# Kernel tuning notes

Hardware: AMD Instinct MI355X
Metric: run time of the kernel (lower is better)

Reference implementation:

```python
import jax, jax.numpy as jnp
import numpy as np

N_NODES = 100000


def gcn_conv(x, src, dst, W, b, n):
    # PyG GCNConv: add self-loops, symmetric deg^-1/2 normalization,
    # linear transform, scatter-add aggregation, bias.
    loops = jnp.arange(n, dtype=src.dtype)
    s = jnp.concatenate([src, loops])
    d = jnp.concatenate([dst, loops])
    deg = jax.ops.segment_sum(jnp.ones_like(s, dtype=x.dtype), d, num_segments=n)
    dinv = jnp.where(deg > 0, jax.lax.rsqrt(deg), 0.0)
    norm = dinv[s] * dinv[d]  # [E+N]
    h = x @ W  # [N, out]
    msgs = h[s] * norm[:, None]  # gather + scale, [E+N, out]
    out = jax.ops.segment_sum(msgs, d, num_segments=n)  # scatter-add
    return out + b


def setup_inputs() -> dict:
    key = jax.random.key(0)
    k1, k2, k3, k4 = jax.random.split(key, 4)
    n, e = N_NODES, 1600000
    cin, chid, cout = 256, 128, 64
    x = jax.random.normal(k1, (n, cin), dtype=jnp.float32)
    edge_index = jax.random.randint(k2, (2, e), 0, n, dtype=jnp.int64)
    W1 = jax.random.normal(k3, (cin, chid), dtype=jnp.float32) * (1.0 / np.sqrt(cin))
    b1 = jnp.zeros((chid,), dtype=jnp.float32)
    W2 = jax.random.normal(k4, (chid, cout), dtype=jnp.float32) * (1.0 / np.sqrt(chid))
    b2 = jnp.zeros((cout,), dtype=jnp.float32)
    return {"x": x, "edge_index": edge_index, "W1": W1, "b1": b1, "W2": W2, "b2": b2}


def reference(x, edge_index, W1, b1, W2, b2):
    n = x.shape[0]
    src, dst = edge_index[0], edge_index[1]
    h = gcn_conv(x, src, dst, W1, b1, n)
    h = jax.nn.relu(h)
    # dropout is identity in eval mode (training=False)
    out = gcn_conv(h, src, dst, W2, b2, n)
    return out
```

## Files before the change

### kernel.cpp

```cpp
#include <hip/hip_runtime.h>


constexpr int NB_SHIFT = 7;
constexpr int NB_MAX   = 1024;
constexpr int BCAP     = 4096;
constexpr int BHIST    = 256;

__global__ __launch_bounds__(256) void k_hist(const int* __restrict__ dst,
                                              int* __restrict__ ghist,
                                              int E, int NB, int epb) {
    __shared__ int h[NB_MAX];
    const int t = threadIdx.x;
    for (int b = t; b < NB; b += 256) h[b] = 0;
    __syncthreads();
    const int e0 = blockIdx.x * epb;
    const int e1 = min(E, e0 + epb);
    for (int e = e0 + t; e < e1; e += 256) atomicAdd(&h[dst[e] >> NB_SHIFT], 1);
    __syncthreads();
    for (int b = t; b < NB; b += 256) ghist[b * gridDim.x + blockIdx.x] = h[b];
}

template <int TPB>
__global__ void k_scanL1(const int* __restrict__ in, int* __restrict__ out,
                         int* __restrict__ bsum, int ntot) {
    __shared__ int s[TPB];
    const int t = threadIdx.x;
    const int g = blockIdx.x * TPB + t;
    int v = (g < ntot) ? in[g] : 0;
    s[t] = v;
    __syncthreads();
    #pragma unroll
    for (int d = 1; d < TPB; d <<= 1) {
        int x = (t >= d) ? s[t - d] : 0;
        __syncthreads();
        s[t] += x;
        __syncthreads();
    }
    if (g < ntot) out[g] = s[t] - v;
    if (t == TPB - 1) bsum[blockIdx.x] = s[t];
}

__global__ void k_scanL2(int* __restrict__ bsum, int nb) {
    __shared__ int s[512];
    const int t = threadIdx.x;
    int v = (t < nb) ? bsum[t] : 0;
    s[t] = v;
    __syncthreads();
    #pragma unroll
    for (int d = 1; d < 512; d <<= 1) {
        int x = (t >= d) ? s[t - d] : 0;
        __syncthreads();
        s[t] += x;
        __syncthreads();
    }
    if (t < nb) bsum[t] = s[t] - v;
}

__global__ __launch_bounds__(256) void k_scatter(const int* __restrict__ src,
                                                 const int* __restrict__ dst,
                                                 const int* __restrict__ scan,
                                                 const int* __restrict__ bsum,
                                                 int2* __restrict__ pairs,
                                                 int E, int NB, int epb) {
    __shared__ int cur[NB_MAX];
    const int t = threadIdx.x;
    const int B = gridDim.x;
    const int blk = blockIdx.x;
    for (int b = t; b < NB; b += 256) {
        int idx = b * B + blk;
        cur[b] = scan[idx] + bsum[idx >> 9];
    }
    __syncthreads();
    const int e0 = blk * epb;
    const int e1 = min(E, e0 + epb);
    for (int e = e0 + t; e < e1; e += 256) {
        int d = dst[e];
        int slot = atomicAdd(&cur[d >> NB_SHIFT], 1);
        pairs[slot] = make_int2(src[e], d);
    }
}

__global__ __launch_bounds__(256) void k_build(const int2* __restrict__ pairs,
                                               const int* __restrict__ scan,
                                               const int* __restrict__ bsum,
                                               int* __restrict__ srcs,
                                               int* __restrict__ off,
                                               float* __restrict__ dinv,
                                               int n, int E, int NB, int B) {
    __shared__ int h[128], loff[128], curs[128];
    __shared__ int sb[BCAP];
    const int t = threadIdx.x;
    const int bk = blockIdx.x;
    const int i0 = bk * B;
    const int base = scan[i0] + bsum[i0 >> 9];
    const int nextbase = (bk + 1 < NB) ? (scan[i0 + B] + bsum[(i0 + B) >> 9]) : E;
    const int count = nextbase - base;
    if (t < 128) h[t] = 0;
    __syncthreads();
    for (int e = t; e < count; e += 256) atomicAdd(&h[pairs[base + e].y & 127], 1);
    __syncthreads();
    if (t < 128) loff[t] = h[t];
    __syncthreads();
    #pragma unroll
    for (int d = 1; d < 128; d <<= 1) {
        int x = 0;
        if (t < 128 && t >= d) x = loff[t - d];
        __syncthreads();
        if (t < 128) loff[t] += x;
        __syncthreads();
    }
    if (t < 128) curs[t] = loff[t] - h[t];
    __syncthreads();
    for (int e = t; e < count; e += 256) {
        int2 p = pairs[base + e];
        int slot = atomicAdd(&curs[p.y & 127], 1);
        if (slot < BCAP) sb[slot] = p.x;
        else srcs[base + slot] = p.x;
    }
    __syncthreads();
    const int lim = min(count, BCAP);
    for (int e = t; e < lim; e += 256) srcs[base + e] = sb[e];
    const int node0 = bk << NB_SHIFT;
    if (t < 128) {
        int node = node0 + t;
        if (node < n) {
            off[node] = base + (loff[t] - h[t]);
            dinv[node] = rsqrtf((float)(h[t] + 1));
        }
    }
    if (bk == 0 && t == 0) off[n] = E;
}

template <int K, int N, int BM, int BK, int TM, int TN>
__global__ __launch_bounds__(256) void k_gemm(const float* __restrict__ A,
                                              const float* __restrict__ B,
                                              float* __restrict__ C, int M) {
    constexpr int BN = N;
    constexpr int NTX = BN / TN;
    __shared__ float As[BM][BK];
    __shared__ float Bs[BK][BN];
    const int t = threadIdx.x;
    const int tx = t % NTX;
    const int ty = t / NTX;
    const int row0 = blockIdx.x * BM;
    float acc[TM][TN] = {};
    for (int kc = 0; kc < K; kc += BK) {
        #pragma unroll
        for (int i = 0; i < BM * BK / (256 * 4); ++i) {
            int f = (t + i * 256) * 4;
            int r = f / BK, kq = f % BK;
            float4 v = make_float4(0.f, 0.f, 0.f, 0.f);
            if (row0 + r < M)
                v = *(const float4*)(A + (size_t)(row0 + r) * K + kc + kq);
            *(float4*)&As[r][kq] = v;
        }
        #pragma unroll
        for (int i = 0; i < BK * BN / (256 * 4); ++i) {
            int f = (t + i * 256) * 4;
            int r = f / BN, c = f % BN;
            *(float4*)&Bs[r][c] = *(const float4*)(B + (size_t)(kc + r) * N + c);
        }
        __syncthreads();
        #pragma unroll
        for (int kk = 0; kk < BK; ++kk) {
            float a[TM], b[TN];
            #pragma unroll
            for (int i = 0; i < TM; ++i) a[i] = As[ty * TM + i][kk];
            #pragma unroll
            for (int j = 0; j < TN; ++j) b[j] = Bs[kk][tx * TN + j];
            #pragma unroll
            for (int i = 0; i < TM; ++i)
                #pragma unroll
                for (int j = 0; j < TN; ++j)
                    acc[i][j] = fmaf(a[i], b[j], acc[i][j]);
        }
        __syncthreads();
    }
    #pragma unroll
    for (int i = 0; i < TM; ++i) {
        int r = row0 + ty * TM + i;
        if (r < M)
            *(float4*)(C + (size_t)r * N + tx * TN) = *(float4*)&acc[i][0];
    }
}

template <int C, bool RELU>
__global__ __launch_bounds__(256) void k_aggregate(
    const float* __restrict__ h, const int* __restrict__ off,
    const int* __restrict__ srcs, const float* __restrict__ dinv,
    const float* __restrict__ bias, float* __restrict__ out, int n) {
    __shared__ float2 stage[256];
    const int tid = threadIdx.x;
    const int lane = tid & 63;
    const int wbase = tid & ~63;
    int wid = (int)((blockIdx.x * (size_t)blockDim.x + tid) >> 6);
    if (wid >= n) return;
    const float di = dinv[wid];
    const int e0 = off[wid], e1 = off[wid + 1];
    if constexpr (C == 128) {
        const float2* hp = (const float2*)h;
        float2 acc = hp[(size_t)wid * 64 + lane];
        acc.x *= di * di;
        acc.y *= di * di;
        for (int e = e0; e < e1; e += 64) {
            int m = e1 - e;
            if (m > 64) m = 64;
            float2 pk = make_float2(0.f, 0.f);
            if (lane < m) {
                int s = srcs[e + lane];
                pk.x = __int_as_float(s);
                pk.y = dinv[s] * di;
            }
            stage[tid] = pk;
            #pragma unroll 4
            for (int j = 0; j < m; ++j) {
                float2 sw = stage[wbase + j];
                int sj = __float_as_int(sw.x);
                float wj = sw.y;
                float2 v = hp[(size_t)sj * 64 + lane];
                acc.x = fmaf(v.x, wj, acc.x);
                acc.y = fmaf(v.y, wj, acc.y);
            }
        }
        float2 bb = ((const float2*)bias)[lane];
        acc.x += bb.x;
        acc.y += bb.y;
        if (RELU) {
            acc.x = fmaxf(acc.x, 0.f);
            acc.y = fmaxf(acc.y, 0.f);
        }
        ((float2*)out)[(size_t)wid * 64 + lane] = acc;
    } else {
        float acc = h[(size_t)wid * C + lane] * di * di;
        for (int e = e0; e < e1; e += 64) {
            int m = e1 - e;
            if (m > 64) m = 64;
            float2 pk = make_float2(0.f, 0.f);
            if (lane < m) {
                int s = srcs[e + lane];
                pk.x = __int_as_float(s);
                pk.y = dinv[s] * di;
            }
            stage[tid] = pk;
            #pragma unroll 4
            for (int j = 0; j < m; ++j) {
                float2 sw = stage[wbase + j];
                int sj = __float_as_int(sw.x);
                float wj = sw.y;
                acc = fmaf(h[(size_t)sj * C + lane], wj, acc);
            }
        }
        acc += bias[lane];
        if (RELU) acc = fmaxf(acc, 0.f);
        out[(size_t)wid * C + lane] = acc;
    }
}

extern "C" void kernel_launch(void* const* d_in, const int* in_sizes, int n_in,
                              void* d_out, int out_size, void* d_ws, size_t ws_size,
                              hipStream_t stream) {
    const float* x  = (const float*)d_in[0];
    const int*   ei = (const int*)d_in[1];
    const float* W1 = (const float*)d_in[2];
    const float* b1 = (const float*)d_in[3];
    const float* W2 = (const float*)d_in[4];
    const float* b2 = (const float*)d_in[5];
    float* out = (float*)d_out;

    const int n = in_sizes[0] / 256;
    const int E = in_sizes[1] / 2;
    const int* src = ei;
    const int* dst = ei + E;

    const int NB  = (n + 127) >> NB_SHIFT;
    const int B   = BHIST;
    const int epb = (E + B - 1) / B;
    const int ntot = NB * B;
    const int gL1 = (ntot + 511) / 512;

    char* p = (char*)d_ws;
    auto alloc = [&](size_t bytes) {
        char* q = p;
        p += (bytes + 255) & ~(size_t)255;
        return q;
    };
    int*   ghist = (int*)alloc((size_t)ntot * 4);
    int*   scan  = (int*)alloc((size_t)ntot * 4);
    int*   bsum  = (int*)alloc(2048);
    int*   off   = (int*)alloc((size_t)(n + 1) * 4);
    float* dinv  = (float*)alloc((size_t)n * 4);
    int*   srcs  = (int*)alloc((size_t)E * 4);
    float* h1    = (float*)alloc((size_t)n * 128 * 4);
    float* h2    = (float*)alloc((size_t)n * 128 * 4);
    int2*  pairs = (int2*)h1;
    float* h3    = h1;

    k_hist<<<B, 256, 0, stream>>>(dst, ghist, E, NB, epb);
    k_scanL1<512><<<gL1, 512, 0, stream>>>(ghist, scan, bsum, ntot);
    k_scanL2<<<1, 512, 0, stream>>>(bsum, gL1);
    k_scatter<<<B, 256, 0, stream>>>(src, dst, scan, bsum, pairs, E, NB, epb);
    k_build<<<NB, 256, 0, stream>>>(pairs, scan, bsum, srcs, off, dinv, n, E, NB, B);

    k_gemm<256, 128, 64, 32, 8, 4><<<(n + 63) / 64, 256, 0, stream>>>(x, W1, h1, n);
    k_aggregate<128, true><<<(n + 3) / 4, 256, 0, stream>>>(h1, off, srcs, dinv, b1, h2, n);

    k_gemm<128, 64, 64, 32, 4, 4><<<(n + 63) / 64, 256, 0, stream>>>(h2, W2, h3, n);
    k_aggregate<64, false><<<(n + 3) / 4, 256, 0, stream>>>(h3, off, srcs, dinv, b2, out, n);
}
```

Baseline: 511.8 us.

## Fuse layer-1 aggregation with layer-2 matmul using shared-memory W2

Adds a kernel that performs the first GCN aggregation (with bias and ReLU) and immediately multiplies each node's hidden row by W2 staged in shared memory, writing the 64-wide layer-2 features directly. This removes the intermediate 128-wide hidden tensor write/read and the separate GEMM launch. The cost is reloading W2 into LDS per block and higher LDS usage per block, which may reduce occupancy for the latency-bound gather loop.

```diff
diff --git a/kernel.cpp b/kernel.cpp
--- a/kernel.cpp
+++ b/kernel.cpp
@@ -184,6 +184,66 @@
     }
 }
 
+__global__ __launch_bounds__(512) void k_agg_mm(
+    const float* __restrict__ h, const int* __restrict__ off,
+    const int* __restrict__ srcs, const float* __restrict__ dinv,
+    const float* __restrict__ b1, const float* __restrict__ W2,
+    float* __restrict__ h3, int n) {
+    __shared__ float W2s[128 * 64];
+    __shared__ float2 stage[512];
+    const int tid = threadIdx.x;
+    #pragma unroll
+    for (int i = 0; i < 4; ++i) {
+        int f = (tid + i * 512) * 4;
+        *(float4*)&W2s[f] = *(const float4*)&W2[f];
+    }
+    __syncthreads();
+    const int lane = tid & 63;
+    const int wbase = tid & ~63;
+    const int wid = blockIdx.x * 8 + (tid >> 6);
+    if (wid >= n) return;
+    const float di = dinv[wid];
+    const int e0 = off[wid], e1 = off[wid + 1];
+    const float2* hp = (const float2*)h;
+    float2 acc = hp[(size_t)wid * 64 + lane];
+    acc.x *= di * di;
+    acc.y *= di * di;
+    for (int e = e0; e < e1; e += 64) {
+        int m = e1 - e;
+        if (m > 64) m = 64;
+        float2 pk = make_float2(0.f, 0.f);
+        if (lane < m) {
+            int s = srcs[e + lane];
+            pk.x = __int_as_float(s);
+            pk.y = dinv[s] * di;
+        }
+        stage[tid] = pk;
+        #pragma unroll 4
+        for (int j = 0; j < m; ++j) {
+            float2 sw = stage[wbase + j];
+            int sj = __float_as_int(sw.x);
+            float wj = sw.y;
+            float2 v = hp[(size_t)sj * 64 + lane];
+            acc.x = fmaf(v.x, wj, acc.x);
+            acc.y = fmaf(v.y, wj, acc.y);
+        }
+    }
+    float2 bb = ((const float2*)b1)[lane];
+    acc.x = fmaxf(acc.x + bb.x, 0.f);
+    acc.y = fmaxf(acc.y + bb.y, 0.f);
+    stage[tid] = acc;
+    const float* row = (const float*)&stage[wbase];
+    float s0 = 0.f, s1 = 0.f, s2 = 0.f, s3 = 0.f;
+    #pragma unroll 8
+    for (int k = 0; k < 128; k += 4) {
+        s0 = fmaf(row[k + 0], W2s[(k + 0) * 64 + lane], s0);
+        s1 = fmaf(row[k + 1], W2s[(k + 1) * 64 + lane], s1);
+        s2 = fmaf(row[k + 2], W2s[(k + 2) * 64 + lane], s2);
+        s3 = fmaf(row[k + 3], W2s[(k + 3) * 64 + lane], s3);
+    }
+    h3[(size_t)wid * 64 + lane] = (s0 + s1) + (s2 + s3);
+}
+
 template <int C, bool RELU>
 __global__ __launch_bounds__(256) void k_aggregate(
     const float* __restrict__ h, const int* __restrict__ off,
@@ -197,63 +257,28 @@
     if (wid >= n) return;
     const float di = dinv[wid];
     const int e0 = off[wid], e1 = off[wid + 1];
-    if constexpr (C == 128) {
-        const float2* hp = (const float2*)h;
-        float2 acc = hp[(size_t)wid * 64 + lane];
-        acc.x *= di * di;
-        acc.y *= di * di;
-        for (int e = e0; e < e1; e += 64) {
-            int m = e1 - e;
-            if (m > 64) m = 64;
-            float2 pk = make_float2(0.f, 0.f);
-            if (lane < m) {
-                int s = srcs[e + lane];
-                pk.x = __int_as_float(s);
-                pk.y = dinv[s] * di;
-            }
-            stage[tid] = pk;
-            #pragma unroll 4
-            for (int j = 0; j < m; ++j) {
-                float2 sw = stage[wbase + j];
-                int sj = __float_as_int(sw.x);
-                float wj = sw.y;
-                float2 v = hp[(size_t)sj * 64 + lane];
-                acc.x = fmaf(v.x, wj, acc.x);
-                acc.y = fmaf(v.y, wj, acc.y);
-            }
-        }
-        float2 bb = ((const float2*)bias)[lane];
-        acc.x += bb.x;
-        acc.y += bb.y;
-        if (RELU) {
-            acc.x = fmaxf(acc.x, 0.f);
-            acc.y = fmaxf(acc.y, 0.f);
-        }
-        ((float2*)out)[(size_t)wid * 64 + lane] = acc;
-    } else {
-        float acc = h[(size_t)wid * C + lane] * di * di;
-        for (int e = e0; e < e1; e += 64) {
-            int m = e1 - e;
-            if (m > 64) m = 64;
-            float2 pk = make_float2(0.f, 0.f);
-            if (lane < m) {
-                int s = srcs[e + lane];
-                pk.x = __int_as_float(s);
-                pk.y = dinv[s] * di;
-            }
-            stage[tid] = pk;
-            #pragma unroll 4
-            for (int j = 0; j < m; ++j) {
-                float2 sw = stage[wbase + j];
-                int sj = __float_as_int(sw.x);
-                float wj = sw.y;
-                acc = fmaf(h[(size_t)sj * C + lane], wj, acc);
-            }
-        }
-        acc += bias[lane];
-        if (RELU) acc = fmaxf(acc, 0.f);
-        out[(size_t)wid * C + lane] = acc;
-    }
+    float acc = h[(size_t)wid * C + lane] * di * di;
+    for (int e = e0; e < e1; e += 64) {
+        int m = e1 - e;
+        if (m > 64) m = 64;
+        float2 pk = make_float2(0.f, 0.f);
+        if (lane < m) {
+            int s = srcs[e + lane];
+            pk.x = __int_as_float(s);
+            pk.y = dinv[s] * di;
+        }
+        stage[tid] = pk;
+        #pragma unroll 4
+        for (int j = 0; j < m; ++j) {
+            float2 sw = stage[wbase + j];
+            int sj = __float_as_int(sw.x);
+            float wj = sw.y;
+            acc = fmaf(h[(size_t)sj * C + lane], wj, acc);
+        }
+    }
+    acc += bias[lane];
+    if (RELU) acc = fmaxf(acc, 0.f);
+    out[(size_t)wid * C + lane] = acc;
 }
 
 extern "C" void kernel_launch(void* const* d_in, const int* in_sizes, int n_in,
@@ -291,9 +316,8 @@
     float* dinv  = (float*)alloc((size_t)n * 4);
     int*   srcs  = (int*)alloc((size_t)E * 4);
     float* h1    = (float*)alloc((size_t)n * 128 * 4);
-    float* h2    = (float*)alloc((size_t)n * 128 * 4);
+    float* h3    = (float*)alloc((size_t)n * 64 * 4);
     int2*  pairs = (int2*)h1;
-    float* h3    = h1;
 
     k_hist<<<B, 256, 0, stream>>>(dst, ghist, E, NB, epb);
     k_scanL1<512><<<gL1, 512, 0, stream>>>(ghist, scan, bsum, ntot);
@@ -302,8 +326,6 @@
     k_build<<<NB, 256, 0, stream>>>(pairs, scan, bsum, srcs, off, dinv, n, E, NB, B);
 
     k_gemm<256, 128, 64, 32, 8, 4><<<(n + 63) / 64, 256, 0, stream>>>(x, W1, h1, n);
-    k_aggregate<128, true><<<(n + 3) / 4, 256, 0, stream>>>(h1, off, srcs, dinv, b1, h2, n);
-
-    k_gemm<128, 64, 64, 32, 4, 4><<<(n + 63) / 64, 256, 0, stream>>>(h2, W2, h3, n);
+    k_agg_mm<<<(n + 7) / 8, 512, 0, stream>>>(h1, off, srcs, dinv, b1, W2, h3, n);
     k_aggregate<64, false><<<(n + 3) / 4, 256, 0, stream>>>(h3, off, srcs, dinv, b2, out, n);
 }
```

Result: no change. 503.4 us (-1.6%).
